# Optimization experiments

Measured on AMD Instinct MI355X. Metric: run time of the kernel, lower is better.

## Reference

```python
import jax, jax.numpy as jnp
import numpy as np

SCALES = (0.9, 1.1)


def resize_bilinear(x, oh, ow):
    """Bilinear resize matching torch F.interpolate(mode='bilinear', align_corners=False).
    x: [B, C, H, W] -> [B, C, oh, ow]."""
    B, C, H, W = x.shape
    if (oh, ow) == (H, W):
        return x
    ys = jnp.clip((jnp.arange(oh, dtype=jnp.float32) + 0.5) * (H / oh) - 0.5, 0.0, H - 1)
    xs = jnp.clip((jnp.arange(ow, dtype=jnp.float32) + 0.5) * (W / ow) - 0.5, 0.0, W - 1)
    y0 = jnp.floor(ys).astype(jnp.int32)
    x0 = jnp.floor(xs).astype(jnp.int32)
    y1 = jnp.minimum(y0 + 1, H - 1)
    x1 = jnp.minimum(x0 + 1, W - 1)
    wy = (ys - y0).astype(x.dtype)[None, None, :, None]
    wx = (xs - x0).astype(x.dtype)[None, None, None, :]
    row = x[:, :, y0, :] * (1 - wy) + x[:, :, y1, :] * wy   # [B,C,oh,W]
    out = row[:, :, :, x0] * (1 - wx) + row[:, :, :, x1] * wx  # [B,C,oh,ow]
    return out


def xcorr_same(feat, filt):
    """F.conv2d cross-correlation with asymmetric 'same' padding as in compute_similarity_scores.
    feat: [1, C, H, W], filt: [N, C, FH, FW] -> [1, N, H, W]."""
    FH, FW = filt.shape[2], filt.shape[3]
    pad = ((FH // 2, (FH - 1) // 2), (FW // 2, (FW - 1) // 2))
    return jax.lax.conv_general_dilated(
        feat, filt, window_strides=(1, 1), padding=pad,
        dimension_numbers=('NCHW', 'OIHW', 'NCHW'))


def scale_boxes(tlbr_np, sh, sw, HF, WF):
    """rescale_box_features: floor top/left, ceil bottom/right, +1 and clamp to feature bounds."""
    t = np.maximum(np.floor(tlbr_np[:, 0] * sh), 0)
    l = np.maximum(np.floor(tlbr_np[:, 1] * sw), 0)
    b = np.minimum(np.ceil(tlbr_np[:, 2] * sh) + 1, HF)
    r = np.minimum(np.ceil(tlbr_np[:, 3] * sw) + 1, WF)
    return np.stack([t, l, b, r], axis=1).astype(np.int32)


def scaled_size(h, w, s):
    hs = int(np.ceil(h * s)); hs = h if hs <= 1 else hs
    ws = int(np.ceil(w * s)); ws = w if ws <= 1 else ws
    return hs, ws


def image_similarities(m3, m4, tlbr_np, img_h, img_w):
    """m3: [512,H3,W3], m4: [1024,H4,W4], tlbr_np: [N,4] int. Returns [6, N, H3, W3]."""
    sims = []
    for feat in (m3, m4):
        C, HF, WF = feat.shape
        sb = scale_boxes(tlbr_np, HF / img_h, WF / img_w, HF, WF)
        crops = [feat[:, t:b, l:r] for t, l, b, r in sb]  # variable-size ROI crops
        mh = max(c.shape[1] for c in crops)
        mw = max(c.shape[2] for c in crops)
        patches = jnp.concatenate(
            [resize_bilinear(c[None], mh, mw) for c in crops], axis=0)  # [N,C,mh,mw]
        sizes = [(mh, mw)] + [scaled_size(mh, mw, s) for s in SCALES]
        for (hs, ws) in sizes:
            filt = resize_bilinear(patches, hs, ws)
            sims.append(xcorr_same(feat[None], filt))  # [1,N,HF,WF]
    # resize_to_uniform_height_width over the 6 similarity maps, then cat on dim0
    mh = max(s.shape[2] for s in sims)
    mw = max(s.shape[3] for s in sims)
    return jnp.concatenate([resize_bilinear(s, mh, mw) for s in sims], axis=0)  # [6,N,mh,mw]


def setup_inputs() -> dict:
    key = jax.random.key(0)
    k3, k4 = jax.random.split(key)
    B, N = 4, 3
    map3 = jax.random.normal(k3, (B, 512, 128, 128), dtype=jnp.float32)
    map4 = jax.random.normal(k4, (B, 1024, 64, 64), dtype=jnp.float32)
    base = np.array([[100, 120, 220, 260],
                     [400,  80, 520, 230],
                     [600, 640, 740, 790]], dtype=np.int32)
    tlbr = jnp.asarray(np.stack([base + 8 * i for i in range(B)], axis=0))  # [B,N,4]
    return {"map3": map3, "map4": map4, "tlbr": tlbr, "img_h": 1024, "img_w": 1024}


def reference(map3, map4, tlbr, img_h, img_w):
    tlbr_np = np.asarray(tlbr)  # box coords are host-side constants (shapes depend on them)
    B = map3.shape[0]
    outs = [image_similarities(map3[i], map4[i], tlbr_np[i], img_h, img_w) for i in range(B)]
    out = jnp.stack(outs, axis=0)          # [B, 6, N, H, W]
    return jnp.transpose(out, (0, 2, 1, 3, 4))  # [B, N, 6, H, W]
```

## Files before the change

### kernel.cpp

```cpp
#include <hip/hip_runtime.h>
#include <math.h>

typedef float  fx4  __attribute__((ext_vector_type(4)));
typedef short  bfx8 __attribute__((ext_vector_type(8)));

__device__ __forceinline__ void bl_w(int o, int O, int I, int& i0, int& i1, float& w) {
    float r = (float)((double)I / (double)O);
    float f = (o + 0.5f) * r - 0.5f;
    f = fminf(fmaxf(f, 0.0f), (float)(I - 1));
    int a = (int)floorf(f);
    i0 = a;
    i1 = min(a + 1, I - 1);
    w = f - (float)a;
}

__device__ __forceinline__ unsigned int bf16rne(float f) {
    unsigned int x = __builtin_bit_cast(unsigned int, f);
    return ((x + 0x7fffu + ((x >> 16) & 1u)) >> 16) & 0xffffu;
}

__global__ void k_meta(const int* __restrict__ tlbr, const int* __restrict__ p_imgh,
                       const int* __restrict__ p_imgw, int B, int N, int ms,
                       int* __restrict__ meta) {
    if (blockIdx.x != 0 || threadIdx.x != 0) return;
    const int HFs[2] = {128, 64};
    const double SC[2] = {0.9, 1.1};
    int img_h = *p_imgh, img_w = *p_imgw;
    for (int b = 0; b < B; ++b)
      for (int lvl = 0; lvl < 2; ++lvl) {
        int HF = HFs[lvl], WF = HFs[lvl];
        double sh = (double)HF / (double)img_h;
        double sw = (double)WF / (double)img_w;
        int* m = meta + (b*2 + lvl)*ms;
        int mh = 0, mw = 0;
        for (int n = 0; n < N; ++n) {
            const int* bx = tlbr + ((size_t)(b*N) + n)*4;
            int t  = max((int)floor((double)bx[0]*sh), 0);
            int l  = max((int)floor((double)bx[1]*sw), 0);
            int bb = min((int)ceil((double)bx[2]*sh) + 1, HF);
            int rr = min((int)ceil((double)bx[3]*sw) + 1, WF);
            int chh = bb - t, cww = rr - l;
            m[2+4*n+0] = t; m[2+4*n+1] = l; m[2+4*n+2] = chh; m[2+4*n+3] = cww;
            mh = max(mh, chh); mw = max(mw, cww);
        }
        m[0] = mh; m[1] = mw;
        int fo = 2 + 4*N;
        m[fo+0] = mh; m[fo+1] = mw;
        for (int s = 0; s < 2; ++s) {
            int hs  = (int)ceil((double)mh * SC[s]); if (hs  <= 1) hs  = mh;
            int wsv = (int)ceil((double)mw * SC[s]); if (wsv <= 1) wsv = mw;
            m[fo+2+2*s] = hs; m[fo+2+2*s+1] = wsv;
        }
      }
}

template<int C, int KH, int KW, int NKYG>
__global__ void k_filters(const float* __restrict__ feat_all, const int* __restrict__ meta,
                          unsigned short* __restrict__ Wswz, int b0, int chunkB,
                          int N, int lvl, int ms, int HF, int WF) {
    constexpr int KT = (C/4)*KW*NKYG;
    long long idx = (long long)blockIdx.x*256 + threadIdx.x;
    long long total = (long long)chunkB * KT * 256;
    if (idx >= total) return;
    int jj = ((int)(idx & 3)) * 2;
    int m  = (int)((idx >> 2) & 15);
    int g  = (int)((idx >> 6) & 3);
    long long rest = idx >> 8;
    int s  = (int)(rest % KT);
    int lb = (int)(rest / KT);
    int kyg = s % NKYG; int s2 = s / NKYG;
    int kx  = s2 % KW;
    int cg  = s2 / KW;
    int c   = cg*4 + g;
    int ky  = kyg*8 + jj;
    unsigned int outv = 0;
    int sc = m / N, n = m - sc*N;
    if (sc < 3) {
        int b = b0 + lb;
        const int* mt = meta + (b*2 + lvl)*ms;
        int mh = mt[0], mw = mt[1];
        int t = mt[2+4*n], l = mt[3+4*n], chh = mt[4+4*n], cww = mt[5+4*n];
        int fo = 2 + 4*N;
        int fh = mt[fo + 2*sc], fw = mt[fo + 2*sc + 1];
        int offy = KH/2 - fh/2, offx = KW/2 - fw/2;
        int fx = kx - offx;
        if (fx >= 0 && fx < fw) {
            const float* src = feat_all + ((size_t)b*C + c)*HF*WF;
            int px0, px1; float wx;
            bl_w(fx, fw, mw, px0, px1, wx);
            int ax0, ax1; float awx; bl_w(px0, mw, cww, ax0, ax1, awx);
            int bx0, bx1; float bwx; bl_w(px1, mw, cww, bx0, bx1, bwx);
            #pragma unroll
            for (int q = 0; q < 2; ++q) {
                int fy = ky + q - offy;
                if (fy >= 0 && fy < fh) {
                    int py0, py1; float wy;
                    bl_w(fy, fh, mh, py0, py1, wy);
                    float pv[2][2];
                    #pragma unroll
                    for (int pi = 0; pi < 2; ++pi) {
                        int py = pi ? py1 : py0;
                        int cy0, cy1; float cwy;
                        bl_w(py, mh, chh, cy0, cy1, cwy);
                        const float* r0 = src + (size_t)(t + cy0)*WF + l;
                        const float* r1 = src + (size_t)(t + cy1)*WF + l;
                        pv[pi][0] = (r0[ax0]*(1.f-cwy) + r1[ax0]*cwy)*(1.f-awx)
                                  + (r0[ax1]*(1.f-cwy) + r1[ax1]*cwy)*awx;
                        pv[pi][1] = (r0[bx0]*(1.f-cwy) + r1[bx0]*cwy)*(1.f-bwx)
                                  + (r0[bx1]*(1.f-cwy) + r1[bx1]*cwy)*bwx;
                    }
                    float v = (pv[0][0]*(1.f-wy) + pv[1][0]*wy)*(1.f-wx)
                            + (pv[0][1]*(1.f-wy) + pv[1][1]*wy)*wx;
                    outv |= bf16rne(v) << (16*q);
                }
            }
        }
    }
    ((unsigned int*)Wswz)[idx] = outv;
}

template<int C, int KS, int KH, int KW, int H, int W, int NKYG, int RSTR, int NCOL, int P>
__global__ __launch_bounds__(256, 4) void k_mfconv(
        const float* __restrict__ feat_all, const unsigned short* __restrict__ Wswz,
        float* __restrict__ part, int b0, int Btot, int N, int nks) {
    constexpr int NDY   = 4;
    constexpr int CHSTR = NCOL*RSTR;
    constexpr int NROWS = KH + (NDY-1)*8;
    constexpr int NRT   = NROWS/4;
    constexpr int NCT   = NCOL/4;
    constexpr int KT    = (C/4)*KW*NKYG;
    constexpr int NFR   = NKYG + NDY - 1;
    __shared__ __align__(16) unsigned short smem[4*CHSTR];

    const int xb  = blockIdx.x;
    const int yb  = blockIdx.y;
    const int zz  = blockIdx.z;
    const int ksp = zz % nks;
    const int lb  = zz / nks;
    const int b   = b0 + lb;
    const int y0  = (yb >> 3)*32 + (yb & 7);
    const int tid = threadIdx.x;
    const int lane = tid & 63;
    const int wv   = tid >> 6;
    const int g    = lane >> 4;
    const int lm   = lane & 15;

    fx4 acc[NDY];
    #pragma unroll
    for (int t = 0; t < NDY; ++t) acc[t] = (fx4){0.f, 0.f, 0.f, 0.f};

    const float* feat = feat_all + (size_t)b * C * H * W;
    const unsigned short* Wlane = Wswz + ((size_t)lb*KT)*512 + lane*8;
    const int bcol = g*CHSTR + (wv*16 + lm)*RSTR;

    const int cg0 = ksp * (KS/4);
    for (int cgl = 0; cgl < KS/4; ++cgl) {
        const int c0 = (cg0 + cgl)*4;
        for (int it = tid; it < 4*NCT*NRT; it += 256) {
            int rt = it % NRT; int t2 = it / NRT;
            int ct = t2 % NCT; int ch = t2 / NCT;
            const float* src = feat + (size_t)(c0 + ch)*H*W;
            int col0 = ct*4, r0 = rt*4;
            int x0 = xb*64 + col0 - P;
            float v[4][4];
            #pragma unroll
            for (int rr = 0; rr < 4; ++rr) {
                int y = y0 + r0 + rr - P;
                bool yok = (y >= 0) && (y < H);
                if (yok && x0 >= 0 && x0 + 3 < W) {
                    const float4 f = *reinterpret_cast<const float4*>(src + (size_t)y*W + x0);
                    v[rr][0] = f.x; v[rr][1] = f.y; v[rr][2] = f.z; v[rr][3] = f.w;
                } else {
                    #pragma unroll
                    for (int j = 0; j < 4; ++j) {
                        int x = x0 + j;
                        v[rr][j] = (yok && x >= 0 && x < W) ? src[(size_t)y*W + x] : 0.f;
                    }
                }
            }
            #pragma unroll
            for (int j = 0; j < 4; ++j) {
                unsigned int lo = bf16rne(v[0][j]) | (bf16rne(v[1][j]) << 16);
                unsigned int hi = bf16rne(v[2][j]) | (bf16rne(v[3][j]) << 16);
                *reinterpret_cast<uint2*>(smem + ch*CHSTR + (col0 + j)*RSTR + r0)
                    = make_uint2(lo, hi);
            }
        }
        __syncthreads();
        const unsigned short* Wc = Wlane + (size_t)((cg0 + cgl)*KW*NKYG)*512;
        for (int kx = 0; kx < KW; ++kx) {
            bfx8 af[NKYG];
            #pragma unroll
            for (int kyg = 0; kyg < NKYG; ++kyg)
                af[kyg] = *reinterpret_cast<const bfx8*>(Wc + (size_t)(kx*NKYG + kyg)*512);
            const unsigned short* bp = smem + bcol + kx*RSTR;
            bfx8 fr[NFR];
            #pragma unroll
            for (int rg = 0; rg < NFR; ++rg)
                fr[rg] = *reinterpret_cast<const bfx8*>(bp + rg*8);
            #pragma unroll
            for (int dy = 0; dy < NDY; ++dy)
                #pragma unroll
                for (int kyg = 0; kyg < NKYG; ++kyg)
                    acc[dy] = __builtin_amdgcn_mfma_f32_16x16x32_bf16(
                        af[kyg], fr[kyg + dy], acc[dy], 0, 0, 0);
        }
        __syncthreads();
    }
    const int x = xb*64 + wv*16 + lm;
    #pragma unroll
    for (int dy = 0; dy < NDY; ++dy) {
        int y = y0 + dy*8;
        #pragma unroll
        for (int r = 0; r < 4; ++r) {
            int m  = g*4 + r;
            int sc = m / N;
            int n  = m - sc*N;
            if (sc < 3) {
                size_t oi = ((((size_t)ksp*Btot + b)*N + n)*3 + sc)*((size_t)H*W)
                          + (size_t)y*W + x;
                part[oi] = acc[dy][r];
            }
        }
    }
}

__global__ void k_reduce3(const float* __restrict__ part, float* __restrict__ out,
                          int B, int N, int nks) {
    int idx = blockIdx.x*256 + threadIdx.x;
    int tot = B*N*3*128*128;
    if (idx >= tot) return;
    int px = idx & 16383;
    int r = idx >> 14;
    int sc = r % 3; r /= 3;
    int n = r % N; int b = r / N;
    size_t stride = (size_t)B*N*3*16384;
    const float* p = part + ((size_t)(b*N + n)*3 + sc)*16384 + px;
    float s = 0.f;
    for (int ks = 0; ks < nks; ++ks) s += p[(size_t)ks*stride];
    out[(((size_t)(b*N + n)*6 + sc) << 14) + px] = s;
}

__global__ void k_upsample_sum(const float* __restrict__ part, float* __restrict__ out,
                               int B, int N, int nks) {
    int idx = blockIdx.x*256 + threadIdx.x;
    int tot = B*N*3*128*128;
    if (idx >= tot) return;
    int x = idx & 127; int r = idx >> 7;
    int y = r & 127; r >>= 7;
    int sc = r % 3; r /= 3;
    int n = r % N; int b = r / N;
    int y0, y1, x0, x1; float wy, wx;
    bl_w(y, 128, 64, y0, y1, wy);
    bl_w(x, 128, 64, x0, x1, wx);
    size_t stride = (size_t)B*N*3*4096;
    const float* p = part + ((size_t)(b*N + n)*3 + sc)*4096;
    float f00 = 0.f, f10 = 0.f, f01 = 0.f, f11 = 0.f;
    for (int ks = 0; ks < nks; ++ks) {
        const float* q = p + (size_t)ks*stride;
        f00 += q[y0*64 + x0]; f10 += q[y1*64 + x0];
        f01 += q[y0*64 + x1]; f11 += q[y1*64 + x1];
    }
    out[((size_t)((b*N + n)*6 + 3 + sc)*128 + y)*128 + x] =
        (f00*(1.f-wy) + f10*wy)*(1.f-wx) + (f01*(1.f-wy) + f11*wy)*wx;
}

extern "C" void kernel_launch(void* const* d_in, const int* in_sizes, int n_in,
                              void* d_out, int out_size, void* d_ws, size_t ws_size,
                              hipStream_t stream) {
    const float* map3 = (const float*)d_in[0];
    const float* map4 = (const float*)d_in[1];
    const int*   tlbr = (const int*)d_in[2];
    const int*   p_imgh = (const int*)d_in[3];
    const int*   p_imgw = (const int*)d_in[4];
    float* out = (float*)d_out;

    const int C3 = 512, H3 = 128, C4 = 1024, H4 = 64;
    int B = in_sizes[0] / (C3 * H3 * H3);
    int N = in_sizes[2] / (B * 4);
    int ms = 2 + 4 * N + 6;
    const int NKS3 = 4, NKS4 = 16;

    char* wsp = (char*)d_ws;
    int* meta = (int*)wsp;
    size_t off = 4096;
    float* part = (float*)(wsp + off);
    size_t part_bytes = (size_t)NKS3 * B * N * 3 * H3 * H3 * 4;
    off += part_bytes;
    unsigned short* Wbuf = (unsigned short*)(wsp + off);
    size_t wavail = (ws_size > off) ? (ws_size - off) : 0;
    size_t wpb = (size_t)(C3/4 * 24 * 3) * 1024;
    int cb = (int)(wavail / wpb); if (cb > B) cb = B; if (cb < 1) cb = 1;

    k_meta<<<1, 1, 0, stream>>>(tlbr, p_imgh, p_imgw, B, N, ms, meta);

    {
        for (int b0 = 0; b0 < B; b0 += cb) {
            int cbn = (cb < B - b0) ? cb : (B - b0);
            long long pr = (long long)cbn * (C3/4 * 24 * 3) * 256;
            k_filters<512,24,24,3><<<(int)((pr + 255) / 256), 256, 0, stream>>>(
                map3, meta, Wbuf, b0, cbn, N, 0, ms, H3, H3);
            dim3 grid(2, 32, cbn * NKS3);
            k_mfconv<512,128,24,24,128,128,3,56,88,12><<<grid, 256, 0, stream>>>(
                map3, Wbuf, part, b0, B, N, NKS3);
        }
        int tot = B * N * 3 * H3 * H3;
        k_reduce3<<<(tot + 255) / 256, 256, 0, stream>>>(part, out, B, N, NKS3);
    }
    {
        for (int b0 = 0; b0 < B; b0 += cb) {
            int cbn = (cb < B - b0) ? cb : (B - b0);
            long long pr = (long long)cbn * (C4/4 * 16 * 2) * 256;
            k_filters<1024,16,16,2><<<(int)((pr + 255) / 256), 256, 0, stream>>>(
                map4, meta, Wbuf, b0, cbn, N, 1, ms, H4, H4);
            dim3 grid(1, 16, cbn * NKS4);
            k_mfconv<1024,64,16,16,64,64,2,40,80,8><<<grid, 256, 0, stream>>>(
                map4, Wbuf, part, b0, B, N, NKS4);
        }
        int tot = B * N * 3 * H3 * H3;
        k_upsample_sum<<<(tot + 255) / 256, 256, 0, stream>>>(part, out, B, N, NKS4);
    }
}
```

Measured before the change: 1.164 ms.

## Remap MFMA K-dimension to kx groups and double output rows per block

The MFMA K-dimension lane groups now span four kx positions of one channel instead of four channels, with the filter and shared-memory layouts reordered to match. Each block now computes 8 output row groups instead of 4, so every weight fragment feeds more MFMAs, and input tiles are staged in 8-row chunks with 128-bit shared stores. The channel split count is doubled and s_setprio is raised around the MFMA bursts to favour the matrix issue. In exchange the kernel needs more accumulator and fragment registers, and the larger split writes more partial sums for the reduction kernels to read.

```diff
diff --git a/kernel.cpp b/kernel.cpp
--- a/kernel.cpp
+++ b/kernel.cpp
@@ -58,7 +58,8 @@
 __global__ void k_filters(const float* __restrict__ feat_all, const int* __restrict__ meta,
                           unsigned short* __restrict__ Wswz, int b0, int chunkB,
                           int N, int lvl, int ms, int HF, int WF) {
-    constexpr int KT = (C/4)*KW*NKYG;
+    constexpr int KWG = KW/4;
+    constexpr int KT  = C*KWG*NKYG;
     long long idx = (long long)blockIdx.x*256 + threadIdx.x;
     long long total = (long long)chunkB * KT * 256;
     if (idx >= total) return;
@@ -69,9 +70,9 @@
     int s  = (int)(rest % KT);
     int lb = (int)(rest / KT);
     int kyg = s % NKYG; int s2 = s / NKYG;
-    int kx  = s2 % KW;
-    int cg  = s2 / KW;
-    int c   = cg*4 + g;
+    int kxg = s2 % KWG;
+    int c   = s2 / KWG;
+    int kx  = kxg*4 + g;
     int ky  = kyg*8 + jj;
     unsigned int outv = 0;
     int sc = m / N, n = m - sc*N;
@@ -119,18 +120,19 @@
     ((unsigned int*)Wswz)[idx] = outv;
 }
 
-template<int C, int KS, int KH, int KW, int H, int W, int NKYG, int RSTR, int NCOL, int P>
+template<int C, int KS, int KH, int KW, int H, int W, int NKYG, int NDY,
+         int CC, int RSTR, int NCOL, int P>
 __global__ __launch_bounds__(256, 4) void k_mfconv(
         const float* __restrict__ feat_all, const unsigned short* __restrict__ Wswz,
         float* __restrict__ part, int b0, int Btot, int N, int nks) {
-    constexpr int NDY   = 4;
+    constexpr int KWG   = KW/4;
     constexpr int CHSTR = NCOL*RSTR;
     constexpr int NROWS = KH + (NDY-1)*8;
-    constexpr int NRT   = NROWS/4;
+    constexpr int NRT   = NROWS/8;
     constexpr int NCT   = NCOL/4;
-    constexpr int KT    = (C/4)*KW*NKYG;
+    constexpr int KT    = C*KWG*NKYG;
     constexpr int NFR   = NKYG + NDY - 1;
-    __shared__ __align__(16) unsigned short smem[4*CHSTR];
+    __shared__ __align__(16) unsigned short smem[CC*CHSTR];
 
     const int xb  = blockIdx.x;
     const int yb  = blockIdx.y;
@@ -138,7 +140,7 @@
     const int ksp = zz % nks;
     const int lb  = zz / nks;
     const int b   = b0 + lb;
-    const int y0  = (yb >> 3)*32 + (yb & 7);
+    const int y0  = (yb >> 3)*(8*NDY) + (yb & 7);
     const int tid = threadIdx.x;
     const int lane = tid & 63;
     const int wv   = tid >> 6;
@@ -151,59 +153,70 @@
 
     const float* feat = feat_all + (size_t)b * C * H * W;
     const unsigned short* Wlane = Wswz + ((size_t)lb*KT)*512 + lane*8;
-    const int bcol = g*CHSTR + (wv*16 + lm)*RSTR;
-
-    const int cg0 = ksp * (KS/4);
-    for (int cgl = 0; cgl < KS/4; ++cgl) {
-        const int c0 = (cg0 + cgl)*4;
-        for (int it = tid; it < 4*NCT*NRT; it += 256) {
+    const int bcol0 = (wv*16 + lm + g)*RSTR;
+
+    for (int cb_ = 0; cb_ < KS; cb_ += CC) {
+        const int c0 = ksp*KS + cb_;
+        for (int it = tid; it < CC*NCT*NRT; it += 256) {
             int rt = it % NRT; int t2 = it / NRT;
             int ct = t2 % NCT; int ch = t2 / NCT;
             const float* src = feat + (size_t)(c0 + ch)*H*W;
-            int col0 = ct*4, r0 = rt*4;
+            int col0 = ct*4, r0 = rt*8;
             int x0 = xb*64 + col0 - P;
-            float v[4][4];
+            float4 f[8];
             #pragma unroll
-            for (int rr = 0; rr < 4; ++rr) {
+            for (int rr = 0; rr < 8; ++rr) {
                 int y = y0 + r0 + rr - P;
                 bool yok = (y >= 0) && (y < H);
                 if (yok && x0 >= 0 && x0 + 3 < W) {
-                    const float4 f = *reinterpret_cast<const float4*>(src + (size_t)y*W + x0);
-                    v[rr][0] = f.x; v[rr][1] = f.y; v[rr][2] = f.z; v[rr][3] = f.w;
+                    f[rr] = *reinterpret_cast<const float4*>(src + (size_t)y*W + x0);
                 } else {
+                    float t4[4];
                     #pragma unroll
                     for (int j = 0; j < 4; ++j) {
                         int x = x0 + j;
-                        v[rr][j] = (yok && x >= 0 && x < W) ? src[(size_t)y*W + x] : 0.f;
+                        t4[j] = (yok && x >= 0 && x < W) ? src[(size_t)y*W + x] : 0.f;
                     }
+                    f[rr] = make_float4(t4[0], t4[1], t4[2], t4[3]);
                 }
             }
             #pragma unroll
             for (int j = 0; j < 4; ++j) {
-                unsigned int lo = bf16rne(v[0][j]) | (bf16rne(v[1][j]) << 16);
-                unsigned int hi = bf16rne(v[2][j]) | (bf16rne(v[3][j]) << 16);
-                *reinterpret_cast<uint2*>(smem + ch*CHSTR + (col0 + j)*RSTR + r0)
-                    = make_uint2(lo, hi);
+                const float* e = (const float*)&f[0];
+                uint4 wv4;
+                wv4.x = bf16rne(((const float*)&f[0])[j]) | (bf16rne(((const float*)&f[1])[j]) << 16);
+                wv4.y = bf16rne(((const float*)&f[2])[j]) | (bf16rne(((const float*)&f[3])[j]) << 16);
+                wv4.z = bf16rne(((const float*)&f[4])[j]) | (bf16rne(((const float*)&f[5])[j]) << 16);
+                wv4.w = bf16rne(((const float*)&f[6])[j]) | (bf16rne(((const float*)&f[7])[j]) << 16);
+                *reinterpret_cast<uint4*>(smem + ch*CHSTR + (col0 + j)*RSTR + r0) = wv4;
+                (void)e;
             }
         }
         __syncthreads();
-        const unsigned short* Wc = Wlane + (size_t)((cg0 + cgl)*KW*NKYG)*512;
-        for (int kx = 0; kx < KW; ++kx) {
-            bfx8 af[NKYG];
-            #pragma unroll
-            for (int kyg = 0; kyg < NKYG; ++kyg)
-                af[kyg] = *reinterpret_cast<const bfx8*>(Wc + (size_t)(kx*NKYG + kyg)*512);
-            const unsigned short* bp = smem + bcol + kx*RSTR;
-            bfx8 fr[NFR];
-            #pragma unroll
-            for (int rg = 0; rg < NFR; ++rg)
-                fr[rg] = *reinterpret_cast<const bfx8*>(bp + rg*8);
-            #pragma unroll
-            for (int dy = 0; dy < NDY; ++dy)
+        #pragma unroll 1
+        for (int ch = 0; ch < CC; ++ch) {
+            const unsigned short* Wc = Wlane + ((size_t)(c0 + ch)*KWG*NKYG)*512;
+            const unsigned short* sb = smem + ch*CHSTR;
+            #pragma unroll 2
+            for (int kxg = 0; kxg < KWG; ++kxg) {
+                bfx8 af[NKYG];
                 #pragma unroll
                 for (int kyg = 0; kyg < NKYG; ++kyg)
-                    acc[dy] = __builtin_amdgcn_mfma_f32_16x16x32_bf16(
-                        af[kyg], fr[kyg + dy], acc[dy], 0, 0, 0);
+                    af[kyg] = *reinterpret_cast<const bfx8*>(Wc + (size_t)(kxg*NKYG + kyg)*512);
+                const unsigned short* bp = sb + bcol0 + kxg*4*RSTR;
+                bfx8 fr[NFR];
+                #pragma unroll
+                for (int rg = 0; rg < NFR; ++rg)
+                    fr[rg] = *reinterpret_cast<const bfx8*>(bp + rg*8);
+                __builtin_amdgcn_s_setprio(1);
+                #pragma unroll
+                for (int dy = 0; dy < NDY; ++dy)
+                    #pragma unroll
+                    for (int kyg = 0; kyg < NKYG; ++kyg)
+                        acc[dy] = __builtin_amdgcn_mfma_f32_16x16x32_bf16(
+                            af[kyg], fr[kyg + dy], acc[dy], 0, 0, 0);
+                __builtin_amdgcn_s_setprio(0);
+            }
         }
         __syncthreads();
     }
@@ -279,7 +292,7 @@
     int B = in_sizes[0] / (C3 * H3 * H3);
     int N = in_sizes[2] / (B * 4);
     int ms = 2 + 4 * N + 6;
-    const int NKS3 = 4, NKS4 = 16;
+    const int NKS3 = 8, NKS4 = 32;
 
     char* wsp = (char*)d_ws;
     int* meta = (int*)wsp;
@@ -289,7 +302,8 @@
     off += part_bytes;
     unsigned short* Wbuf = (unsigned short*)(wsp + off);
     size_t wavail = (ws_size > off) ? (ws_size - off) : 0;
-    size_t wpb = (size_t)(C3/4 * 24 * 3) * 1024;
+    size_t wpb = (size_t)(512/4 * 6 * 3 * 4) * 1024;
+    wpb = (size_t)9216 * 1024;
     int cb = (int)(wavail / wpb); if (cb > B) cb = B; if (cb < 1) cb = 1;
 
     k_meta<<<1, 1, 0, stream>>>(tlbr, p_imgh, p_imgw, B, N, ms, meta);
@@ -297,11 +311,11 @@
     {
         for (int b0 = 0; b0 < B; b0 += cb) {
             int cbn = (cb < B - b0) ? cb : (B - b0);
-            long long pr = (long long)cbn * (C3/4 * 24 * 3) * 256;
+            long long pr = (long long)cbn * 9216 * 256;
             k_filters<512,24,24,3><<<(int)((pr + 255) / 256), 256, 0, stream>>>(
                 map3, meta, Wbuf, b0, cbn, N, 0, ms, H3, H3);
-            dim3 grid(2, 32, cbn * NKS3);
-            k_mfconv<512,128,24,24,128,128,3,56,88,12><<<grid, 256, 0, stream>>>(
+            dim3 grid(2, 16, cbn * NKS3);
+            k_mfconv<512,64,24,24,128,128,3,8,2,88,88,12><<<grid, 256, 0, stream>>>(
                 map3, Wbuf, part, b0, B, N, NKS3);
         }
         int tot = B * N * 3 * H3 * H3;
@@ -310,11 +324,11 @@
     {
         for (int b0 = 0; b0 < B; b0 += cb) {
             int cbn = (cb < B - b0) ? cb : (B - b0);
-            long long pr = (long long)cbn * (C4/4 * 16 * 2) * 256;
+            long long pr = (long long)cbn * 8192 * 256;
             k_filters<1024,16,16,2><<<(int)((pr + 255) / 256), 256, 0, stream>>>(
                 map4, meta, Wbuf, b0, cbn, N, 1, ms, H4, H4);
-            dim3 grid(1, 16, cbn * NKS4);
-            k_mfconv<1024,64,16,16,64,64,2,40,80,8><<<grid, 256, 0, stream>>>(
+            dim3 grid(1, 8, cbn * NKS4);
+            k_mfconv<1024,32,16,16,64,64,2,8,2,72,80,8><<<grid, 256, 0, stream>>>(
                 map4, Wbuf, part, b0, B, N, NKS4);
         }
         int tot = B * N * 3 * H3 * H3;
```

Result: faster. 975.1 us (-16.2%).
